# Optimization experiments

Hardware: AMD Instinct MI355X
Metric: run time of the kernel (lower is better)

Reference implementation:

```python
import jax, jax.numpy as jnp
import numpy as np

B, H, S, D = 4, 12, 2048, 64


def setup_inputs() -> dict:
    key = jax.random.key(0)
    k1, k2, k3 = jax.random.split(key, 3)
    keys = jax.random.normal(k1, (B, H, S, D), dtype=jnp.float32)
    queries = jax.random.normal(k2, (B, H, S, D), dtype=jnp.float32)
    values = jax.random.normal(k3, (B, H, S, D), dtype=jnp.float32)
    return {"keys": keys, "queries": queries, "values": values}


def reference(keys, queries, values):
    d_k = keys.shape[-1]
    # scores: [B, H, S, S]
    scores = jnp.einsum("bhqd,bhkd->bhqk", queries, keys) / jnp.sqrt(jnp.asarray(d_k, dtype=scores_dtype(queries)))
    s = scores.shape[-1]
    causal = jnp.triu(jnp.ones((s, s), dtype=bool), k=1)  # True above diagonal -> masked
    scores = jnp.where(causal, -jnp.inf, scores)
    attn = jax.nn.softmax(scores, axis=-1)
    return jnp.einsum("bhqk,bhkd->bhqd", attn, values)


def scores_dtype(x):
    return x.dtype
```

## Files before the change

kernel.cpp:

```cpp
#include <hip/hip_runtime.h>
#include <hip/hip_bf16.h>

#define B_SZ 4
#define H_SZ 12
#define S_LEN 2048
#define DH 64
#define KT 64
#define NQT (S_LEN / 64)
#define M2 9.0f

typedef _Float16 half8 __attribute__((ext_vector_type(8)));
typedef _Float16 half4v __attribute__((ext_vector_type(4)));
typedef float f32x4 __attribute__((ext_vector_type(4)));

__device__ __forceinline__ int gk_swz(int row) { return ((row & 3) << 1) | ((row >> 3) & 1); }
__device__ __forceinline__ int gv_swz(int d) { return (d & 7) ^ ((d >> 3) & 7); }

#define GLOAD_LDS16(gp, lp)                                                              \
    __builtin_amdgcn_global_load_lds(                                                    \
        (const __attribute__((address_space(1))) void*)(gp),                             \
        (__attribute__((address_space(3))) void*)(lp), 16, 0, 0)

__global__ __launch_bounds__(256) void cvt_pre(
    const float* __restrict__ Kg, const float* __restrict__ Vg,
    _Float16* __restrict__ wsK, _Float16* __restrict__ wsV)
{
    const int blk = blockIdx.x;
    const size_t gbase = (size_t)blk * (64 * 64);
    const int t = threadIdx.x;

    __shared__ float vt[64 * 65];

#pragma unroll
    for (int i = 0; i < 4; ++i) {
        int f = t + 256 * i;
        int row = f >> 4, c4 = (f & 15) << 2;
        float4 v = *(const float4*)(Vg + gbase + row * 64 + c4);
        vt[row * 65 + c4 + 0] = v.x; vt[row * 65 + c4 + 1] = v.y;
        vt[row * 65 + c4 + 2] = v.z; vt[row * 65 + c4 + 3] = v.w;
    }

#pragma unroll
    for (int i = 0; i < 2; ++i) {
        int u = t + 256 * i;
        int row = u >> 3, p = u & 7;
        int s = p ^ gk_swz(row);
        float4 x = *(const float4*)(Kg + gbase + row * 64 + s * 8);
        float4 y = *(const float4*)(Kg + gbase + row * 64 + s * 8 + 4);
        half8 h;
        h[0]=(_Float16)x.x; h[1]=(_Float16)x.y; h[2]=(_Float16)x.z; h[3]=(_Float16)x.w;
        h[4]=(_Float16)y.x; h[5]=(_Float16)y.y; h[6]=(_Float16)y.z; h[7]=(_Float16)y.w;
        *(half8*)&wsK[(size_t)blk * 4096 + row * 64 + p * 8] = h;
    }

    __syncthreads();

#pragma unroll
    for (int i = 0; i < 2; ++i) {
        int u = t + 256 * i;
        int d = u >> 3, p = u & 7;
        int s = p ^ gv_swz(d);
        half8 h;
#pragma unroll
        for (int e = 0; e < 8; ++e) h[e] = (_Float16)vt[(s * 8 + e) * 65 + d];
        *(half8*)&wsV[(size_t)blk * 4096 + d * 64 + p * 8] = h;
    }
}

__global__ __launch_bounds__(256, 5) void fa_fwd_ws(
    const _Float16* __restrict__ wsK,
    const _Float16* __restrict__ wsV,
    const float* __restrict__ Qg,
    float* __restrict__ Og)
{
    const int bh = blockIdx.x;
    const int qt = (NQT - 1) - blockIdx.y;
    const size_t base = (size_t)bh * S_LEN * DH;

    const int tid  = threadIdx.x;
    const int wave = tid >> 6;
    const int lane = tid & 63;
    const int l16  = lane & 15;
    const int quad = lane >> 4;

    __shared__ __align__(16) _Float16 Klds[2][64 * 64];
    __shared__ __align__(16) _Float16 Vlds[2][64 * 64];

    const int r0 = qt * 64 + wave * 16;

    const float qs = 0.125f * 1.44269504f;
    half8 qf[2];
    {
        const float* pq = Qg + base + (size_t)(r0 + l16) * DH + quad * 8;
#pragma unroll
        for (int c = 0; c < 2; ++c) {
            float4 x = *(const float4*)(pq + c * 32);
            float4 y = *(const float4*)(pq + c * 32 + 4);
            half8 f;
            f[0]=(_Float16)(x.x*qs); f[1]=(_Float16)(x.y*qs); f[2]=(_Float16)(x.z*qs); f[3]=(_Float16)(x.w*qs);
            f[4]=(_Float16)(y.x*qs); f[5]=(_Float16)(y.y*qs); f[6]=(_Float16)(y.z*qs); f[7]=(_Float16)(y.w*qs);
            qf[c] = f;
        }
    }

    auto stage = [&](int bb, int tile) {
        const size_t toff = ((size_t)(bh * 32 + tile)) << 13;
        const char* kS = (const char*)wsK + toff + wave * 2048 + lane * 16;
        const char* vS = (const char*)wsV + toff + wave * 2048 + lane * 16;
        char* kL = (char*)&Klds[bb][0] + wave * 2048;
        char* vL = (char*)&Vlds[bb][0] + wave * 2048;
        GLOAD_LDS16(kS,        kL);
        GLOAD_LDS16(kS + 1024, kL + 1024);
        GLOAD_LDS16(vS,        vL);
        GLOAD_LDS16(vS + 1024, vL + 1024);
    };

    f32x4 oacc[4];
#pragma unroll
    for (int t = 0; t < 4; ++t) oacc[t] = f32x4{0.f,0.f,0.f,0.f};
    f32x4 lacc = f32x4{0.f,0.f,0.f,0.f};
    const half8 ones = {(_Float16)1.f,(_Float16)1.f,(_Float16)1.f,(_Float16)1.f,
                        (_Float16)1.f,(_Float16)1.f,(_Float16)1.f,(_Float16)1.f};

    const int kr0    = ((l16 >> 2) << 3) + (l16 & 3);
    const int qrow64 = wave * 16 + l16;
    const int klq    = quad * 8;

    auto kfrag = [&](int b, int c, int t) -> half8 {
        int row = kr0 + ((t & 1) << 2) + ((t >> 1) << 5);
        int p = (((c << 2) + quad) ^ gk_swz(row));
        return *(const half8*)&Klds[b][row * 64 + (p << 3)];
    };
    auto vfrag = [&](int b, int c, int t) -> half8 {
        int d = l16 + 16 * t;
        int p = (((c << 2) + quad) ^ gv_swz(d));
        return *(const half8*)&Vlds[b][d * 64 + (p << 3)];
    };
    auto mask_diag = [&](f32x4* sc) {
#pragma unroll
        for (int t = 0; t < 4; ++t)
#pragma unroll
            for (int r = 0; r < 4; ++r)
                if (klq + ((t & 1) << 2) + ((t >> 1) << 5) + r > qrow64) sc[t][r] = -1e30f;
    };
    auto exp_all = [&](f32x4* sc) {
#pragma unroll
        for (int t = 0; t < 4; ++t)
#pragma unroll
            for (int r = 0; r < 4; ++r)
                sc[t][r] = __builtin_amdgcn_exp2f(sc[t][r] - M2);
    };
    auto pack_pa = [&](const f32x4* sc, int c) -> half8 {
        half8 pa;
        const f32x4 s0 = sc[2 * c], s1 = sc[2 * c + 1];
        pa[0] = (_Float16)s0[0]; pa[1] = (_Float16)s0[1];
        pa[2] = (_Float16)s0[2]; pa[3] = (_Float16)s0[3];
        pa[4] = (_Float16)s1[0]; pa[5] = (_Float16)s1[1];
        pa[6] = (_Float16)s1[2]; pa[7] = (_Float16)s1[3];
        return pa;
    };

    auto do_tile = [&](int b, bool diag) {
        f32x4 sc[4];
#pragma unroll
        for (int t = 0; t < 4; ++t) sc[t] = f32x4{0.f,0.f,0.f,0.f};
        __builtin_amdgcn_s_setprio(1);
#pragma unroll
        for (int c = 0; c < 2; ++c)
#pragma unroll
            for (int t = 0; t < 4; ++t)
                sc[t] = __builtin_amdgcn_mfma_f32_16x16x32_f16(kfrag(b, c, t), qf[c], sc[t], 0, 0, 0);
        __builtin_amdgcn_s_setprio(0);
        if (diag) mask_diag(sc);
        exp_all(sc);
#pragma unroll
        for (int c = 0; c < 2; ++c) {
            half8 pa = pack_pa(sc, c);
            __builtin_amdgcn_s_setprio(1);
            lacc = __builtin_amdgcn_mfma_f32_16x16x32_f16(ones, pa, lacc, 0, 0, 0);
#pragma unroll
            for (int t = 0; t < 4; ++t)
                oacc[t] = __builtin_amdgcn_mfma_f32_16x16x32_f16(vfrag(b, c, t), pa, oacc[t], 0, 0, 0);
            __builtin_amdgcn_s_setprio(0);
        }
    };

    const int niter = qt + 1;
    int b = 0;
    stage(0, 0);
    for (int it = 0; it < niter; ++it) {
        __syncthreads();
        if (it + 1 < niter) stage(b ^ 1, it + 1);
        asm volatile("" ::: "memory");
        do_tile(b, it == niter - 1);
        b ^= 1;
    }

    const float il = 1.0f / lacc[0];
#pragma unroll
    for (int t = 0; t < 4; ++t)
        *(f32x4*)(Og + base + (size_t)(r0 + l16) * DH + 16 * t + quad * 4) = oacc[t] * il;
}

__global__ __launch_bounds__(256, 3) void fa_fwd_legacy(
    const float* __restrict__ Kg,
    const float* __restrict__ Qg,
    const float* __restrict__ Vg,
    float* __restrict__ Og)
{
    const int bh = blockIdx.x;
    const int j  = blockIdx.y;
    const size_t base = (size_t)bh * S_LEN * DH;

    const int tid  = threadIdx.x;
    const int wave = tid >> 6;
    const int lane = tid & 63;
    const int l16  = lane & 15;
    const int quad = lane >> 4;

    __shared__ __align__(16) _Float16 Klds[2][KT * 72];
    __shared__ __align__(16) _Float16 Vlds[2][DH * 64];

    const int rlo = j * 64 + wave * 16;
    const int rhi = (NQT - 1 - j) * 64 + wave * 16;

    const float qs = 0.125f * 1.44269504f;
    half8 qlo[2], qhi[2];
    {
        const float* plo = Qg + base + (size_t)(rlo + l16) * DH + quad * 8;
        const float* phi = Qg + base + (size_t)(rhi + l16) * DH + quad * 8;
#pragma unroll
        for (int c = 0; c < 2; ++c) {
            float4 x = *(const float4*)(plo + c * 32);
            float4 y = *(const float4*)(plo + c * 32 + 4);
            half8 f;
            f[0]=(_Float16)(x.x*qs); f[1]=(_Float16)(x.y*qs); f[2]=(_Float16)(x.z*qs); f[3]=(_Float16)(x.w*qs);
            f[4]=(_Float16)(y.x*qs); f[5]=(_Float16)(y.y*qs); f[6]=(_Float16)(y.z*qs); f[7]=(_Float16)(y.w*qs);
            qlo[c] = f;
            x = *(const float4*)(phi + c * 32);
            y = *(const float4*)(phi + c * 32 + 4);
            f[0]=(_Float16)(x.x*qs); f[1]=(_Float16)(x.y*qs); f[2]=(_Float16)(x.z*qs); f[3]=(_Float16)(x.w*qs);
            f[4]=(_Float16)(y.x*qs); f[5]=(_Float16)(y.y*qs); f[6]=(_Float16)(y.z*qs); f[7]=(_Float16)(y.w*qs);
            qhi[c] = f;
        }
    }

    float4 kreg[4];
    float  vreg[16];

    auto load_tile = [&](int kv0) {
#pragma unroll
        for (int i = 0; i < 4; ++i) {
            int f = tid + 256 * i;
            kreg[i] = *(const float4*)(Kg + base + (size_t)(kv0 + (f >> 4)) * DH + ((f & 15) << 2));
        }
        const float* vp = Vg + base + (size_t)(kv0 + wave * 16) * DH + lane;
#pragma unroll
        for (int jj = 0; jj < 16; ++jj) vreg[jj] = vp[jj * DH];
    };
    auto cvt_store = [&](int b) {
#pragma unroll
        for (int i = 0; i < 4; ++i) {
            int f = tid + 256 * i;
            half4v hk = {(_Float16)kreg[i].x, (_Float16)kreg[i].y,
                         (_Float16)kreg[i].z, (_Float16)kreg[i].w};
            *(half4v*)&Klds[b][(f >> 4) * 72 + ((f & 15) << 2)] = hk;
        }
        half8 lo, hi;
#pragma unroll
        for (int jj = 0; jj < 8; ++jj) { lo[jj] = (_Float16)vreg[jj]; hi[jj] = (_Float16)vreg[jj + 8]; }
        _Float16* vrow = &Vlds[b][lane * 64];
        *(half8*)&vrow[(((2 * wave + 0) ^ (lane & 7)) << 3)] = lo;
        *(half8*)&vrow[(((2 * wave + 1) ^ (lane & 7)) << 3)] = hi;
    };

    f32x4 olo[4], ohi[4];
#pragma unroll
    for (int t = 0; t < 4; ++t) { olo[t] = f32x4{0.f,0.f,0.f,0.f}; ohi[t] = f32x4{0.f,0.f,0.f,0.f}; }
    f32x4 llo = f32x4{0.f,0.f,0.f,0.f}, lhi = f32x4{0.f,0.f,0.f,0.f};
    const half8 ones = {(_Float16)1.f,(_Float16)1.f,(_Float16)1.f,(_Float16)1.f,
                        (_Float16)1.f,(_Float16)1.f,(_Float16)1.f,(_Float16)1.f};

    const int kr0    = ((l16 >> 2) << 3) + (l16 & 3);
    const int qrow64 = wave * 16 + l16;
    const int klq    = quad * 8;

    auto kfrag = [&](int b, int c, int t) -> half8 {
        return *(const half8*)&Klds[b][(kr0 + ((t & 1) << 2) + ((t >> 1) << 5)) * 72 + c * 32 + quad * 8];
    };
    auto vfrag = [&](int b, int c, int t) -> half8 {
        int d = l16 + 16 * t;
        return *(const half8*)&Vlds[b][d * 64 + ((((c << 2) + quad) ^ (d & 7)) << 3)];
    };
    auto mask_diag = [&](f32x4* sc) {
#pragma unroll
        for (int t = 0; t < 4; ++t)
#pragma unroll
            for (int r = 0; r < 4; ++r)
                if (klq + ((t & 1) << 2) + ((t >> 1) << 5) + r > qrow64) sc[t][r] = -1e30f;
    };
    auto exp_all = [&](f32x4* sc) {
#pragma unroll
        for (int t = 0; t < 4; ++t)
#pragma unroll
            for (int r = 0; r < 4; ++r)
                sc[t][r] = __builtin_amdgcn_exp2f(sc[t][r] - M2);
    };
    auto pack_pa = [&](const f32x4* sc, int c) -> half8 {
        half8 pa;
        const f32x4 s0 = sc[2 * c], s1 = sc[2 * c + 1];
        pa[0] = (_Float16)s0[0]; pa[1] = (_Float16)s0[1];
        pa[2] = (_Float16)s0[2]; pa[3] = (_Float16)s0[3];
        pa[4] = (_Float16)s1[0]; pa[5] = (_Float16)s1[1];
        pa[6] = (_Float16)s1[2]; pa[7] = (_Float16)s1[3];
        return pa;
    };

    auto do_single = [&](int b, const half8* qf, f32x4* oacc, f32x4& lacc, bool diag) {
        f32x4 sc[4];
#pragma unroll
        for (int t = 0; t < 4; ++t) sc[t] = f32x4{0.f,0.f,0.f,0.f};
#pragma unroll
        for (int c = 0; c < 2; ++c)
#pragma unroll
            for (int t = 0; t < 4; ++t)
                sc[t] = __builtin_amdgcn_mfma_f32_16x16x32_f16(kfrag(b, c, t), qf[c], sc[t], 0, 0, 0);
        if (diag) mask_diag(sc);
        exp_all(sc);
#pragma unroll
        for (int c = 0; c < 2; ++c) {
            half8 pa = pack_pa(sc, c);
            lacc = __builtin_amdgcn_mfma_f32_16x16x32_f16(ones, pa, lacc, 0, 0, 0);
#pragma unroll
            for (int t = 0; t < 4; ++t)
                oacc[t] = __builtin_amdgcn_mfma_f32_16x16x32_f16(vfrag(b, c, t), pa, oacc[t], 0, 0, 0);
        }
    };

    auto do_dual = [&](int b, bool dlo) {
        f32x4 sh[4], sl[4];
#pragma unroll
        for (int t = 0; t < 4; ++t) { sh[t] = f32x4{0.f,0.f,0.f,0.f}; sl[t] = f32x4{0.f,0.f,0.f,0.f}; }
#pragma unroll
        for (int c = 0; c < 2; ++c)
#pragma unroll
            for (int t = 0; t < 4; ++t) {
                half8 kf = kfrag(b, c, t);
                sh[t] = __builtin_amdgcn_mfma_f32_16x16x32_f16(kf, qhi[c], sh[t], 0, 0, 0);
                sl[t] = __builtin_amdgcn_mfma_f32_16x16x32_f16(kf, qlo[c], sl[t], 0, 0, 0);
            }
        if (dlo) mask_diag(sl);
        exp_all(sh);
        exp_all(sl);
#pragma unroll
        for (int c = 0; c < 2; ++c) {
            half8 ph = pack_pa(sh, c);
            half8 pl = pack_pa(sl, c);
            lhi = __builtin_amdgcn_mfma_f32_16x16x32_f16(ones, ph, lhi, 0, 0, 0);
            llo = __builtin_amdgcn_mfma_f32_16x16x32_f16(ones, pl, llo, 0, 0, 0);
#pragma unroll
            for (int t = 0; t < 4; ++t) {
                half8 vb = vfrag(b, c, t);
                ohi[t] = __builtin_amdgcn_mfma_f32_16x16x32_f16(vb, ph, ohi[t], 0, 0, 0);
                olo[t] = __builtin_amdgcn_mfma_f32_16x16x32_f16(vb, pl, olo[t], 0, 0, 0);
            }
        }
    };

    const int niter = NQT - j;
    load_tile(0);
    int b = 0;
    for (int it = 0; it < niter; ++it) {
        cvt_store(b);
        __syncthreads();
        if (it + 1 < niter) load_tile((it + 1) * KT);
        asm volatile("" ::: "memory");
        if (it <= j) do_dual(b, it == j);
        else         do_single(b, qhi, ohi, lhi, it == niter - 1);
        b ^= 1;
    }

    const float il = 1.0f / llo[0];
    const float ih = 1.0f / lhi[0];
#pragma unroll
    for (int t = 0; t < 4; ++t) {
        *(f32x4*)(Og + base + (size_t)(rlo + l16) * DH + 16 * t + quad * 4) = olo[t] * il;
        *(f32x4*)(Og + base + (size_t)(rhi + l16) * DH + 16 * t + quad * 4) = ohi[t] * ih;
    }
}

extern "C" void kernel_launch(void* const* d_in, const int* in_sizes, int n_in,
                              void* d_out, int out_size, void* d_ws, size_t ws_size,
                              hipStream_t stream) {
    const float* K = (const float*)d_in[0];
    const float* Q = (const float*)d_in[1];
    const float* V = (const float*)d_in[2];
    float* O = (float*)d_out;

    const size_t halfs_per_tensor = (size_t)B_SZ * H_SZ * S_LEN * DH;
    const size_t ws_needed = 2 * halfs_per_tensor * sizeof(_Float16);

    if (d_ws != nullptr && ws_size >= ws_needed) {
        _Float16* wsK = (_Float16*)d_ws;
        _Float16* wsV = wsK + halfs_per_tensor;
        cvt_pre<<<dim3(B_SZ * H_SZ * NQT), dim3(256), 0, stream>>>(K, V, wsK, wsV);
        dim3 grid(B_SZ * H_SZ, NQT);
        fa_fwd_ws<<<grid, dim3(256), 0, stream>>>(wsK, wsV, Q, O);
    } else {
        dim3 grid(B_SZ * H_SZ, NQT / 2);
        fa_fwd_legacy<<<grid, dim3(256), 0, stream>>>(K, Q, V, O);
    }
}
```

Before: 148.2 us.

## Single-buffer V tile in LDS, staging it mid-iteration, and raise occupancy target

V is now held in one LDS buffer instead of two. Its load is issued at the start of each iteration and overlaps the QK^T MFMAs and the softmax exp, with a second barrier placed before the PV MFMAs. The LDS saving and a launch-bounds change from 5 to 6 blocks per CU aim for higher occupancy. In exchange, each iteration gains an extra barrier, and the V load latency is only hidden by the score computation rather than a full iteration.

Measured after the change: 148.1 us. About the same (-0.1%).

```diff
diff --git a/kernel.cpp b/kernel.cpp
--- a/kernel.cpp
+++ b/kernel.cpp
@@ -67,7 +67,7 @@
     }
 }
 
-__global__ __launch_bounds__(256, 5) void fa_fwd_ws(
+__global__ __launch_bounds__(256, 6) void fa_fwd_ws(
     const _Float16* __restrict__ wsK,
     const _Float16* __restrict__ wsV,
     const float* __restrict__ Qg,
@@ -84,7 +84,7 @@
     const int quad = lane >> 4;
 
     __shared__ __align__(16) _Float16 Klds[2][64 * 64];
-    __shared__ __align__(16) _Float16 Vlds[2][64 * 64];
+    __shared__ __align__(16) _Float16 Vlds[64 * 64];
 
     const int r0 = qt * 64 + wave * 16;
 
@@ -103,14 +103,17 @@
         }
     }
 
-    auto stage = [&](int bb, int tile) {
+    auto stageK = [&](int bb, int tile) {
         const size_t toff = ((size_t)(bh * 32 + tile)) << 13;
         const char* kS = (const char*)wsK + toff + wave * 2048 + lane * 16;
-        const char* vS = (const char*)wsV + toff + wave * 2048 + lane * 16;
         char* kL = (char*)&Klds[bb][0] + wave * 2048;
-        char* vL = (char*)&Vlds[bb][0] + wave * 2048;
         GLOAD_LDS16(kS,        kL);
         GLOAD_LDS16(kS + 1024, kL + 1024);
+    };
+    auto stageV = [&](int tile) {
+        const size_t toff = ((size_t)(bh * 32 + tile)) << 13;
+        const char* vS = (const char*)wsV + toff + wave * 2048 + lane * 16;
+        char* vL = (char*)&Vlds[0] + wave * 2048;
         GLOAD_LDS16(vS,        vL);
         GLOAD_LDS16(vS + 1024, vL + 1024);
     };
@@ -131,24 +134,10 @@
         int p = (((c << 2) + quad) ^ gk_swz(row));
         return *(const half8*)&Klds[b][row * 64 + (p << 3)];
     };
-    auto vfrag = [&](int b, int c, int t) -> half8 {
+    auto vfrag = [&](int c, int t) -> half8 {
         int d = l16 + 16 * t;
         int p = (((c << 2) + quad) ^ gv_swz(d));
-        return *(const half8*)&Vlds[b][d * 64 + (p << 3)];
-    };
-    auto mask_diag = [&](f32x4* sc) {
-#pragma unroll
-        for (int t = 0; t < 4; ++t)
-#pragma unroll
-            for (int r = 0; r < 4; ++r)
-                if (klq + ((t & 1) << 2) + ((t >> 1) << 5) + r > qrow64) sc[t][r] = -1e30f;
-    };
-    auto exp_all = [&](f32x4* sc) {
-#pragma unroll
-        for (int t = 0; t < 4; ++t)
-#pragma unroll
-            for (int r = 0; r < 4; ++r)
-                sc[t][r] = __builtin_amdgcn_exp2f(sc[t][r] - M2);
+        return *(const half8*)&Vlds[d * 64 + (p << 3)];
     };
     auto pack_pa = [&](const f32x4* sc, int c) -> half8 {
         half8 pa;
@@ -160,7 +149,15 @@
         return pa;
     };
 
-    auto do_tile = [&](int b, bool diag) {
+    const int niter = qt + 1;
+    int b = 0;
+    stageK(0, 0);
+    for (int it = 0; it < niter; ++it) {
+        __syncthreads();
+        stageV(it);
+        if (it + 1 < niter) stageK(b ^ 1, it + 1);
+        asm volatile("" ::: "memory");
+
         f32x4 sc[4];
 #pragma unroll
         for (int t = 0; t < 4; ++t) sc[t] = f32x4{0.f,0.f,0.f,0.f};
@@ -171,28 +168,33 @@
             for (int t = 0; t < 4; ++t)
                 sc[t] = __builtin_amdgcn_mfma_f32_16x16x32_f16(kfrag(b, c, t), qf[c], sc[t], 0, 0, 0);
         __builtin_amdgcn_s_setprio(0);
-        if (diag) mask_diag(sc);
-        exp_all(sc);
-#pragma unroll
-        for (int c = 0; c < 2; ++c) {
-            half8 pa = pack_pa(sc, c);
-            __builtin_amdgcn_s_setprio(1);
-            lacc = __builtin_amdgcn_mfma_f32_16x16x32_f16(ones, pa, lacc, 0, 0, 0);
+        if (it == niter - 1) {
 #pragma unroll
             for (int t = 0; t < 4; ++t)
-                oacc[t] = __builtin_amdgcn_mfma_f32_16x16x32_f16(vfrag(b, c, t), pa, oacc[t], 0, 0, 0);
-            __builtin_amdgcn_s_setprio(0);
-        }
-    };
-
-    const int niter = qt + 1;
-    int b = 0;
-    stage(0, 0);
-    for (int it = 0; it < niter; ++it) {
+#pragma unroll
+                for (int r = 0; r < 4; ++r)
+                    if (klq + ((t & 1) << 2) + ((t >> 1) << 5) + r > qrow64) sc[t][r] = -1e30f;
+        }
+#pragma unroll
+        for (int t = 0; t < 4; ++t)
+#pragma unroll
+            for (int r = 0; r < 4; ++r)
+                sc[t][r] = __builtin_amdgcn_exp2f(sc[t][r] - M2);
+        half8 pa0 = pack_pa(sc, 0);
+        half8 pa1 = pack_pa(sc, 1);
+
         __syncthreads();
-        if (it + 1 < niter) stage(b ^ 1, it + 1);
-        asm volatile("" ::: "memory");
-        do_tile(b, it == niter - 1);
+
+        __builtin_amdgcn_s_setprio(1);
+        lacc = __builtin_amdgcn_mfma_f32_16x16x32_f16(ones, pa0, lacc, 0, 0, 0);
+#pragma unroll
+        for (int t = 0; t < 4; ++t)
+            oacc[t] = __builtin_amdgcn_mfma_f32_16x16x32_f16(vfrag(0, t), pa0, oacc[t], 0, 0, 0);
+        lacc = __builtin_amdgcn_mfma_f32_16x16x32_f16(ones, pa1, lacc, 0, 0, 0);
+#pragma unroll
+        for (int t = 0; t < 4; ++t)
+            oacc[t] = __builtin_amdgcn_mfma_f32_16x16x32_f16(vfrag(1, t), pa1, oacc[t], 0, 0, 0);
+        __builtin_amdgcn_s_setprio(0);
         b ^= 1;
     }
 
```
